# Performance work log

Measured on AMD Instinct MI355X. Metric: run time of the kernel, lower is better.

Reference implementation:

```python
import jax, jax.numpy as jnp
import numpy as np

N, F_IN, E = 50000, 256, 1000000
UNITS, HEADS, LAYERS, OUT = 32, 8, 2, 64
D = UNITS * HEADS  # 256


def setup_inputs() -> dict:
    key = jax.random.key(0)
    ks = jax.random.split(key, 12)
    node_states = jax.random.normal(ks[0], (1, N, F_IN), dtype=jnp.float32)
    # edges sorted by source column (required by the tf.repeat/bincount trick)
    src = jnp.sort(jax.random.randint(ks[1], (E,), 0, N, dtype=jnp.int32))
    dst = jax.random.randint(ks[2], (E,), 0, N, dtype=jnp.int32)
    edges = jnp.stack([src, dst], axis=-1)[None]  # [1, E, 2]
    edge_weights = jax.random.uniform(ks[3], (1, E), dtype=jnp.float32)
    pos_cls = jax.random.randint(ks[4], (1, 128), 0, N, dtype=jnp.int32)
    s = 0.05
    Wp = jax.random.normal(ks[5], (F_IN, D), dtype=jnp.float32) * s
    bp = jnp.zeros((D,), dtype=jnp.float32)
    Wk = jax.random.normal(ks[6], (LAYERS, HEADS, D, UNITS), dtype=jnp.float32) * s
    Wa = jax.random.normal(ks[7], (LAYERS, HEADS, 2 * UNITS, 1), dtype=jnp.float32) * s
    Wo = jax.random.normal(ks[8], (D, OUT), dtype=jnp.float32) * s
    bo = jnp.zeros((OUT,), dtype=jnp.float32)
    return {
        "node_states": node_states, "edges": edges, "edge_weights": edge_weights,
        "pos_cls": pos_cls, "Wp": Wp, "bp": bp, "Wk": Wk, "Wa": Wa,
        "Wo": Wo, "bo": bo,
    }


def _gat_head(x, src, dst, ew, W, a, n_nodes):
    xt = x @ W  # [N, U]
    # edge features: concat(src_feat, dst_feat) scaled by edge weight
    ef = jnp.concatenate([xt[src], xt[dst]], axis=-1) * ew[:, None]  # [E, 2U]
    s = jax.nn.leaky_relu((ef @ a)[:, 0], negative_slope=0.2)        # [E]
    s = jnp.exp(jnp.clip(s, -2.0, 2.0))
    ssum = jax.ops.segment_sum(s, src, num_segments=n_nodes)          # [N]
    norm = s / ssum[src]
    return jax.ops.segment_sum(xt[dst] * norm[:, None], src, num_segments=n_nodes)


def reference(node_states, edges, edge_weights, pos_cls, Wp, bp, Wk, Wa, Wo, bo):
    x0 = node_states[0]        # [N, F_in]
    e = edges[0]               # [E, 2]
    ew = edge_weights[0]       # [E]
    src, dst = e[:, 0], e[:, 1]
    n_nodes = x0.shape[0]
    x = jax.nn.relu(x0 @ Wp + bp)  # [N, D]
    n_layers, n_heads = Wk.shape[0], Wk.shape[1]
    for l in range(n_layers):
        heads = [_gat_head(x, src, dst, ew, Wk[l, h], Wa[l, h], n_nodes)
                 for h in range(n_heads)]
        mh = jax.nn.relu(jnp.concatenate(heads, axis=-1))  # [N, D]
        x = mh + x  # residual
    out = x @ Wo + bo
    return out[None]  # [1, N, OUT]
```

## Files before the change

### kernel.cpp

```cpp
#include <hip/hip_runtime.h>
#include <hip/hip_bf16.h>
#include <math.h>

#define N_NODES 50000
#define F_DIM 256
#define NE 1000000
#define N_HEADS 8
#define M_PAD 50048

typedef __attribute__((ext_vector_type(8))) short short8;
typedef __attribute__((ext_vector_type(4))) float floatx4;
typedef __attribute__((ext_vector_type(2))) float floatx2;

__device__ __forceinline__ void load16_lds(const void* g, void* l) {
    __builtin_amdgcn_global_load_lds(
        (const __attribute__((address_space(1))) unsigned int*)(unsigned long long)g,
        (__attribute__((address_space(3))) unsigned int*)(unsigned int)(unsigned long long)l,
        16, 0, 0);
}

__device__ __forceinline__ unsigned int pack2bf(float a, float b) {
    __hip_bfloat16 t0 = __float2bfloat16(a), t1 = __float2bfloat16(b);
    unsigned short u0, u1;
    __builtin_memcpy(&u0, &t0, 2);
    __builtin_memcpy(&u1, &t1, 2);
    return (unsigned int)u0 | ((unsigned int)u1 << 16);
}

__device__ __forceinline__ float bf_lo(unsigned int u) {
    return __uint_as_float(u << 16);
}
__device__ __forceinline__ float bf_hi(unsigned int u) {
    return __uint_as_float(u & 0xffff0000u);
}

__device__ __forceinline__ unsigned int pack4fp8(float x, float y, float z,
                                                 float w) {
    int v = __builtin_amdgcn_cvt_pk_fp8_f32(x, y, 0, false);
    v = __builtin_amdgcn_cvt_pk_fp8_f32(z, w, v, true);
    return (unsigned int)v;
}

__global__ __launch_bounds__(256) void prep_kernel(
    const float* __restrict__ node_states, const int* __restrict__ edges,
    const float* __restrict__ ew, const float* __restrict__ Wp,
    const float* __restrict__ Wk, const float* __restrict__ Wo,
    __hip_bfloat16* __restrict__ xt16, int2* __restrict__ edata,
    __hip_bfloat16* __restrict__ wpT, __hip_bfloat16* __restrict__ wkT,
    __hip_bfloat16* __restrict__ woT, int* __restrict__ row_start) {
    const int b = blockIdx.x;
    const int tid = threadIdx.x;
    if (b < 12500) {
        const size_t i = ((size_t)b * 256 + tid) * 4;
        const float4 v = *(const float4*)(node_states + i);
        uint2 pk;
        pk.x = pack2bf(v.x, v.y);
        pk.y = pack2bf(v.z, v.w);
        *(uint2*)((unsigned short*)xt16 + i) = pk;
    } else if (b < 16407) {
        const int e = (b - 12500) * 256 + tid;
        if (e < NE) {
            int2 d;
            d.x = edges[2 * e + 1];
            d.y = __float_as_int(ew[e]);
            edata[e] = d;
        }
    } else if (b < 17239) {
        const int wb = b - 16407;
        if (wb < 256) {
            int idx = wb * 256 + tid;
            int n = idx >> 8, k = idx & 255;
            wpT[idx] = __float2bfloat16(Wp[k * 256 + n]);
        } else if (wb < 768) {
            int idx = (wb - 256) * 256 + tid;
            int l = idx >> 16, n = (idx >> 8) & 255, k = idx & 255;
            int h = n >> 5, u = n & 31;
            wkT[idx] = __float2bfloat16(Wk[(((l * 8 + h) * 256) + k) * 32 + u]);
        } else {
            int idx = (wb - 768) * 256 + tid;
            int n = idx >> 8, k = idx & 255;
            woT[idx] = __float2bfloat16(Wo[k * 64 + n]);
        }
    } else {
        const int i = (b - 17239) * 256 + tid;
        if (i > N_NODES) return;
        if (i == N_NODES) { row_start[N_NODES] = NE; return; }
        int lo = 0, hi = NE;
        while (lo < hi) {
            int mid = (lo + hi) >> 1;
            if (edges[2 * mid] < i) lo = mid + 1; else hi = mid;
        }
        row_start[i] = lo;
    }
}

template <bool BIAS_RELU, bool FP8OUT>
__global__ __launch_bounds__(256) void gemm_mfma(
    const __hip_bfloat16* __restrict__ A16, const __hip_bfloat16* __restrict__ BT,
    const float* __restrict__ bias, void* __restrict__ Y) {
    __shared__ __align__(16) short lA[128 * 32];
    __shared__ __align__(16) short lB[128 * 32];
    const int tid = threadIdx.x;
    const int row0 = blockIdx.x * 128;
    const int n0 = blockIdx.y * 128;
    const int w = tid >> 6, l = tid & 63;
    const int wr = w >> 1, wc = w & 1;

    const __hip_bfloat16* gA = A16 + (size_t)(row0 + (tid >> 2)) * 256 + (tid & 3) * 8;
    const __hip_bfloat16* gB = BT + (size_t)(n0 + (tid >> 2)) * 256 + (tid & 3) * 8;
    short* dA = lA + tid * 8;
    short* dB = lB + tid * 8;

    floatx4 acc[4][4] = {};

    const short* pa = lA + (wr * 64 + (l & 15)) * 32 + (l >> 4) * 8;
    const short* pb = lB + (wc * 64 + (l & 15)) * 32 + (l >> 4) * 8;

    for (int kk = 0; kk < 8; ++kk) {
        const int ko = kk * 32;
        load16_lds(gA + ko, dA);
        load16_lds(gA + 64 * 256 + ko, dA + 256 * 8);
        load16_lds(gB + ko, dB);
        load16_lds(gB + 64 * 256 + ko, dB + 256 * 8);
        __syncthreads();
        short8 af[4], bf[4];
#pragma unroll
        for (int t = 0; t < 4; ++t) {
            af[t] = *(const short8*)(pa + t * 16 * 32);
            bf[t] = *(const short8*)(pb + t * 16 * 32);
        }
#pragma unroll
        for (int mt = 0; mt < 4; ++mt)
#pragma unroll
            for (int nt = 0; nt < 4; ++nt)
                acc[mt][nt] = __builtin_amdgcn_mfma_f32_16x16x32_bf16(
                    bf[nt], af[mt], acc[mt][nt], 0, 0, 0);
        __syncthreads();
    }

    const int m_base = row0 + wr * 64 + (l & 15);
    const int n_base = n0 + wc * 64 + ((l >> 4) << 2);
#pragma unroll
    for (int mt = 0; mt < 4; ++mt) {
        const int m = m_base + mt * 16;
        if (m >= N_NODES) continue;
#pragma unroll
        for (int nt = 0; nt < 4; ++nt) {
            const int n = n_base + nt * 16;
            floatx4 v = acc[mt][nt];
            if (BIAS_RELU) {
                const float4 bb = *(const float4*)(bias + n);
                v.x = fmaxf(v.x + bb.x, 0.f);
                v.y = fmaxf(v.y + bb.y, 0.f);
                v.z = fmaxf(v.z + bb.z, 0.f);
                v.w = fmaxf(v.w + bb.w, 0.f);
            }
            if constexpr (FP8OUT) {
                *((unsigned int*)Y + (((size_t)m << 8) + n >> 2)) =
                    pack4fp8(v.x, v.y, v.z, v.w);
            } else {
                uint2 pk;
                pk.x = pack2bf(v.x, v.y);
                pk.y = pack2bf(v.z, v.w);
                *(uint2*)((unsigned short*)Y + ((size_t)m << 8) + n) = pk;
            }
        }
    }
}

__global__ __launch_bounds__(256) void gemm_mfma_out(
    const __hip_bfloat16* __restrict__ A16, const __hip_bfloat16* __restrict__ BT,
    const float* __restrict__ bias, float* __restrict__ out) {
    __shared__ __align__(16) short lA[128 * 32];
    __shared__ __align__(16) short lB[64 * 32];
    const int tid = threadIdx.x;
    const int row0 = blockIdx.x * 128;
    const int w = tid >> 6, l = tid & 63;

    const __hip_bfloat16* gA = A16 + (size_t)(row0 + (tid >> 2)) * 256 + (tid & 3) * 8;
    const __hip_bfloat16* gB = BT + (size_t)(tid >> 2) * 256 + (tid & 3) * 8;
    short* dA = lA + tid * 8;
    short* dB = lB + tid * 8;

    floatx4 acc[2][4] = {};

    const short* pa = lA + (w * 32 + (l & 15)) * 32 + (l >> 4) * 8;
    const short* pb = lB + (l & 15) * 32 + (l >> 4) * 8;

    for (int kk = 0; kk < 8; ++kk) {
        const int ko = kk * 32;
        load16_lds(gA + ko, dA);
        load16_lds(gA + 64 * 256 + ko, dA + 256 * 8);
        load16_lds(gB + ko, dB);
        __syncthreads();
        short8 af[2], bf[4];
#pragma unroll
        for (int t = 0; t < 2; ++t) af[t] = *(const short8*)(pa + t * 16 * 32);
#pragma unroll
        for (int t = 0; t < 4; ++t) bf[t] = *(const short8*)(pb + t * 16 * 32);
#pragma unroll
        for (int mt = 0; mt < 2; ++mt)
#pragma unroll
            for (int nt = 0; nt < 4; ++nt)
                acc[mt][nt] = __builtin_amdgcn_mfma_f32_16x16x32_bf16(
                    bf[nt], af[mt], acc[mt][nt], 0, 0, 0);
        __syncthreads();
    }

    const int m_base = row0 + w * 32 + (l & 15);
    const int n_base = (l >> 4) << 2;
#pragma unroll
    for (int mt = 0; mt < 2; ++mt) {
        const int m = m_base + mt * 16;
        if (m >= N_NODES) continue;
#pragma unroll
        for (int nt = 0; nt < 4; ++nt) {
            const int n = n_base + nt * 16;
            const float4 bb = *(const float4*)(bias + n);
            floatx4 v = acc[mt][nt];
            float4 o = {v.x + bb.x, v.y + bb.y, v.z + bb.z, v.w + bb.w};
            *(float4*)(&out[(size_t)m * 64 + n]) = o;
        }
    }
}

__global__ __launch_bounds__(256) void alpha_kernel(
    const unsigned int* __restrict__ xt8, const float* __restrict__ Wa_l,
    float* __restrict__ a_src, float* __restrict__ a_dst) {
    const int tid = threadIdx.x;
    const int node =
        __builtin_amdgcn_readfirstlane(blockIdx.x * 4 + (tid >> 6));
    const int l = tid & 63;
    const int h = l >> 3;
    const unsigned int u = xt8[(size_t)node * 64 + l];
    const floatx2 f01 = __builtin_amdgcn_cvt_pk_f32_fp8(u, false);
    const floatx2 f23 = __builtin_amdgcn_cvt_pk_f32_fp8(u, true);
    const float4 wa = *(const float4*)(Wa_l + h * 64 + (l & 7) * 4);
    const float4 wb = *(const float4*)(Wa_l + h * 64 + 32 + (l & 7) * 4);
    float p1 = f01.x * wa.x + f01.y * wa.y + f23.x * wa.z + f23.y * wa.w;
    float p2 = f01.x * wb.x + f01.y * wb.y + f23.x * wb.z + f23.y * wb.w;
#pragma unroll
    for (int off = 4; off > 0; off >>= 1) {
        p1 += __shfl_down(p1, off, 8);
        p2 += __shfl_down(p2, off, 8);
    }
    if ((l & 7) == 0) {
        a_src[node * N_HEADS + h] = p1;
        a_dst[node * N_HEADS + h] = p2;
    }
}

__device__ __forceinline__ float edge_score(float asrc, float ad, float w) {
    float sp = (asrc + ad) * w;
    sp = (sp >= 0.f) ? sp : 0.2f * sp;
    sp = fminf(fmaxf(sp, -2.f), 2.f);
    return __expf(sp);
}

#define ACC8(u, s)                                               \
    {                                                            \
        const floatx2 f01 = __builtin_amdgcn_cvt_pk_f32_fp8(u, false); \
        const floatx2 f23 = __builtin_amdgcn_cvt_pk_f32_fp8(u, true);  \
        a0 = fmaf(f01.x, s, a0);                                 \
        a1 = fmaf(f01.y, s, a1);                                 \
        a2 = fmaf(f23.x, s, a2);                                 \
        a3 = fmaf(f23.y, s, a3);                                 \
    }

__global__ __launch_bounds__(256) void edge_kernel(
    const unsigned long long* __restrict__ edata,
    const int* __restrict__ row_start, const unsigned int* __restrict__ xt8,
    const float* __restrict__ a_src, const float* __restrict__ a_dst,
    __hip_bfloat16* __restrict__ xb16) {
    const int tid = threadIdx.x;
    const int node =
        __builtin_amdgcn_readfirstlane(blockIdx.x * 4 + (tid >> 6));
    const int l = tid & 63;
    const int h = l >> 3;
    const float asrc = a_src[node * N_HEADS + h];
    const int e0 = row_start[node], e1 = row_start[node + 1];

    unsigned long long* xrow =
        (unsigned long long*)((unsigned short*)xb16 + (size_t)node * 256 +
                              l * 4);
    const unsigned long long xin = __builtin_nontemporal_load(xrow);

    float a0 = 0.f, a1 = 0.f, a2 = 0.f, a3 = 0.f, ssum = 0.f;
    int e = e0;
    for (; e + 4 <= e1; e += 4) {
        const unsigned long long ed0 = __builtin_nontemporal_load(edata + e);
        const unsigned long long ed1 = __builtin_nontemporal_load(edata + e + 1);
        const unsigned long long ed2 = __builtin_nontemporal_load(edata + e + 2);
        const unsigned long long ed3 = __builtin_nontemporal_load(edata + e + 3);
        const int d0 = (int)(unsigned int)ed0;
        const int d1 = (int)(unsigned int)ed1;
        const int d2 = (int)(unsigned int)ed2;
        const int d3 = (int)(unsigned int)ed3;
        const float w0 = __uint_as_float((unsigned int)(ed0 >> 32));
        const float w1 = __uint_as_float((unsigned int)(ed1 >> 32));
        const float w2 = __uint_as_float((unsigned int)(ed2 >> 32));
        const float w3 = __uint_as_float((unsigned int)(ed3 >> 32));
        const float s0 = edge_score(asrc, a_dst[d0 * N_HEADS + h], w0);
        const float s1 = edge_score(asrc, a_dst[d1 * N_HEADS + h], w1);
        const float s2 = edge_score(asrc, a_dst[d2 * N_HEADS + h], w2);
        const float s3 = edge_score(asrc, a_dst[d3 * N_HEADS + h], w3);
        const unsigned int u0 = xt8[(size_t)d0 * 64 + l];
        const unsigned int u1 = xt8[(size_t)d1 * 64 + l];
        const unsigned int u2 = xt8[(size_t)d2 * 64 + l];
        const unsigned int u3 = xt8[(size_t)d3 * 64 + l];
        ACC8(u0, s0);
        ACC8(u1, s1);
        ACC8(u2, s2);
        ACC8(u3, s3);
        ssum += (s0 + s1) + (s2 + s3);
    }
    for (; e < e1; ++e) {
        const unsigned long long ed = __builtin_nontemporal_load(edata + e);
        const int d = (int)(unsigned int)ed;
        const float w = __uint_as_float((unsigned int)(ed >> 32));
        const float s = edge_score(asrc, a_dst[d * N_HEADS + h], w);
        const unsigned int u = xt8[(size_t)d * 64 + l];
        ACC8(u, s);
        ssum += s;
    }
    const float inv = (e1 > e0) ? 1.f / ssum : 0.f;
    const unsigned int xlo = (unsigned int)xin;
    const unsigned int xhi = (unsigned int)(xin >> 32);
    const float c0 = bf_lo(xlo) + fmaxf(a0 * inv, 0.f);
    const float c1 = bf_hi(xlo) + fmaxf(a1 * inv, 0.f);
    const float c2 = bf_lo(xhi) + fmaxf(a2 * inv, 0.f);
    const float c3 = bf_hi(xhi) + fmaxf(a3 * inv, 0.f);
    const unsigned long long pk =
        (unsigned long long)pack2bf(c0, c1) |
        ((unsigned long long)pack2bf(c2, c3) << 32);
    __builtin_nontemporal_store(pk, xrow);
}

extern "C" void kernel_launch(void* const* d_in, const int* in_sizes, int n_in,
                              void* d_out, int out_size, void* d_ws,
                              size_t ws_size, hipStream_t stream) {
    const float* node_states = (const float*)d_in[0];
    const int* edges = (const int*)d_in[1];
    const float* ew = (const float*)d_in[2];
    const float* Wp = (const float*)d_in[4];
    const float* bp = (const float*)d_in[5];
    const float* Wk = (const float*)d_in[6];
    const float* Wa = (const float*)d_in[7];
    const float* Wo = (const float*)d_in[8];
    const float* bo = (const float*)d_in[9];
    float* out = (float*)d_out;

    char* ws = (char*)d_ws;
    __hip_bfloat16* xb16 = (__hip_bfloat16*)ws; ws += (size_t)M_PAD * 256 * 2;
    __hip_bfloat16* xt16 = (__hip_bfloat16*)ws; ws += (size_t)M_PAD * 256 * 2;
    unsigned int* xt8 = (unsigned int*)ws;      ws += (size_t)M_PAD * 256;
    int2* edata = (int2*)ws;                    ws += (size_t)NE * 8;
    float* a_src = (float*)ws;                  ws += (size_t)N_NODES * N_HEADS * 4;
    float* a_dst = (float*)ws;                  ws += (size_t)N_NODES * N_HEADS * 4;
    __hip_bfloat16* wpT = (__hip_bfloat16*)ws;  ws += 65536 * 2;
    __hip_bfloat16* wkT = (__hip_bfloat16*)ws;  ws += 131072 * 2;
    __hip_bfloat16* woT = (__hip_bfloat16*)ws;  ws += 16384 * 2;
    int* row_st = (int*)ws;

    prep_kernel<<<17435, 256, 0, stream>>>(node_states, edges, ew, Wp, Wk, Wo,
                                           xt16, edata, wpT, wkT, woT, row_st);

    gemm_mfma<true, false><<<dim3((N_NODES + 127) / 128, 2), 256, 0, stream>>>(
        xt16, wpT, bp, xb16);

    gemm_mfma<false, true><<<dim3((N_NODES + 127) / 128, 2), 256, 0, stream>>>(
        xb16, wkT, nullptr, xt8);
    alpha_kernel<<<N_NODES / 4, 256, 0, stream>>>(xt8, Wa, a_src, a_dst);
    edge_kernel<<<N_NODES / 4, 256, 0, stream>>>(
        (const unsigned long long*)edata, row_st, xt8, a_src, a_dst, xb16);

    gemm_mfma<false, true><<<dim3((N_NODES + 127) / 128, 2), 256, 0, stream>>>(
        xb16, wkT + 65536, nullptr, xt8);
    alpha_kernel<<<N_NODES / 4, 256, 0, stream>>>(xt8, Wa + 512, a_src, a_dst);
    edge_kernel<<<N_NODES / 4, 256, 0, stream>>>(
        (const unsigned long long*)edata, row_st, xt8, a_src, a_dst, xb16);

    gemm_mfma_out<<<(N_NODES + 127) / 128, 256, 0, stream>>>(xb16, woT, bo, out);
}
```

Before: 306.8 us.

## Fuse attention logits into GEMM epilogue and split edge loop across half-waves

Removes the separate alpha kernel by computing per-head source and destination attention logits in the GEMM epilogue from fp32 accumulators, using cross-lane shuffles. The edge kernel now has each half-wave handle alternating groups of four edges, with every lane gathering 8 fp8 features (uint2) instead of 4. The two halves are combined with an xor shuffle. This drops one launch and one full read of xt8 per layer and doubles the edge-level parallelism per wave. The cost is extra epilogue work, predicated padding edges, and logits computed from unrounded accumulators instead of fp8 values, which slightly changes numerics.

New measurement: 314.4 us. +2.5%, slower.

```diff
diff --git a/kernel.cpp b/kernel.cpp
--- a/kernel.cpp
+++ b/kernel.cpp
@@ -11,6 +11,7 @@
 typedef __attribute__((ext_vector_type(8))) short short8;
 typedef __attribute__((ext_vector_type(4))) float floatx4;
 typedef __attribute__((ext_vector_type(2))) float floatx2;
+typedef __attribute__((ext_vector_type(4))) unsigned int uintx4;
 
 __device__ __forceinline__ void load16_lds(const void* g, void* l) {
     __builtin_amdgcn_global_load_lds(
@@ -94,10 +95,12 @@
     }
 }
 
-template <bool BIAS_RELU, bool FP8OUT>
+template <bool BIAS_RELU, bool FP8OUT, bool ALPHA>
 __global__ __launch_bounds__(256) void gemm_mfma(
     const __hip_bfloat16* __restrict__ A16, const __hip_bfloat16* __restrict__ BT,
-    const float* __restrict__ bias, void* __restrict__ Y) {
+    const float* __restrict__ bias, void* __restrict__ Y,
+    const float* __restrict__ Wa_l, float* __restrict__ a_srcO,
+    float* __restrict__ a_dstO) {
     __shared__ __align__(16) short lA[128 * 32];
     __shared__ __align__(16) short lB[128 * 32];
     const int tid = threadIdx.x;
@@ -156,13 +159,60 @@
                 v.w = fmaxf(v.w + bb.w, 0.f);
             }
             if constexpr (FP8OUT) {
-                *((unsigned int*)Y + (((size_t)m << 8) + n >> 2)) =
+                *((unsigned int*)Y + ((((size_t)m << 8) + n) >> 2)) =
                     pack4fp8(v.x, v.y, v.z, v.w);
             } else {
                 uint2 pk;
                 pk.x = pack2bf(v.x, v.y);
                 pk.y = pack2bf(v.z, v.w);
                 *(uint2*)((unsigned short*)Y + ((size_t)m << 8) + n) = pk;
+            }
+        }
+    }
+
+    if constexpr (ALPHA) {
+        const int lg = l >> 4;
+        float4 wS[2][2], wD[2][2];
+#pragma unroll
+        for (int hl = 0; hl < 2; ++hl) {
+            const int h = (n0 >> 5) + wc * 2 + hl;
+#pragma unroll
+            for (int p = 0; p < 2; ++p) {
+                wS[hl][p] = *(const float4*)(Wa_l + h * 64 + p * 16 + lg * 4);
+                wD[hl][p] =
+                    *(const float4*)(Wa_l + h * 64 + 32 + p * 16 + lg * 4);
+            }
+        }
+        float aS[4][2], aD[4][2];
+#pragma unroll
+        for (int mt = 0; mt < 4; ++mt)
+#pragma unroll
+            for (int hl = 0; hl < 2; ++hl) {
+                float s = 0.f, d = 0.f;
+#pragma unroll
+                for (int p = 0; p < 2; ++p) {
+                    const floatx4 v = acc[mt][2 * hl + p];
+                    const float4 ws = wS[hl][p], wd = wD[hl][p];
+                    s += v.x * ws.x + v.y * ws.y + v.z * ws.z + v.w * ws.w;
+                    d += v.x * wd.x + v.y * wd.y + v.z * wd.z + v.w * wd.w;
+                }
+                s += __shfl_xor(s, 16);
+                s += __shfl_xor(s, 32);
+                d += __shfl_xor(d, 16);
+                d += __shfl_xor(d, 32);
+                aS[mt][hl] = s;
+                aD[mt][hl] = d;
+            }
+        if (lg == 0) {
+#pragma unroll
+            for (int mt = 0; mt < 4; ++mt) {
+                const int m = m_base + mt * 16;
+#pragma unroll
+                for (int hl = 0; hl < 2; ++hl) {
+                    const int h = (n0 >> 5) + wc * 2 + hl;
+                    a_srcO[(size_t)m * 8 + h] = aS[mt][hl];
+                    a_dstO[(size_t)m * 8 + h] = aD[mt][hl];
+                }
             }
         }
     }
@@ -224,32 +274,6 @@
     }
 }
 
-__global__ __launch_bounds__(256) void alpha_kernel(
-    const unsigned int* __restrict__ xt8, const float* __restrict__ Wa_l,
-    float* __restrict__ a_src, float* __restrict__ a_dst) {
-    const int tid = threadIdx.x;
-    const int node =
-        __builtin_amdgcn_readfirstlane(blockIdx.x * 4 + (tid >> 6));
-    const int l = tid & 63;
-    const int h = l >> 3;
-    const unsigned int u = xt8[(size_t)node * 64 + l];
-    const floatx2 f01 = __builtin_amdgcn_cvt_pk_f32_fp8(u, false);
-    const floatx2 f23 = __builtin_amdgcn_cvt_pk_f32_fp8(u, true);
-    const float4 wa = *(const float4*)(Wa_l + h * 64 + (l & 7) * 4);
-    const float4 wb = *(const float4*)(Wa_l + h * 64 + 32 + (l & 7) * 4);
-    float p1 = f01.x * wa.x + f01.y * wa.y + f23.x * wa.z + f23.y * wa.w;
-    float p2 = f01.x * wb.x + f01.y * wb.y + f23.x * wb.z + f23.y * wb.w;
-#pragma unroll
-    for (int off = 4; off > 0; off >>= 1) {
-        p1 += __shfl_down(p1, off, 8);
-        p2 += __shfl_down(p2, off, 8);
-    }
-    if ((l & 7) == 0) {
-        a_src[node * N_HEADS + h] = p1;
-        a_dst[node * N_HEADS + h] = p2;
-    }
-}
-
 __device__ __forceinline__ float edge_score(float asrc, float ad, float w) {
     float sp = (asrc + ad) * w;
     sp = (sp >= 0.f) ? sp : 0.2f * sp;
@@ -257,83 +281,81 @@
     return __expf(sp);
 }
 
-#define ACC8(u, s)                                               \
-    {                                                            \
-        const floatx2 f01 = __builtin_amdgcn_cvt_pk_f32_fp8(u, false); \
-        const floatx2 f23 = __builtin_amdgcn_cvt_pk_f32_fp8(u, true);  \
-        a0 = fmaf(f01.x, s, a0);                                 \
-        a1 = fmaf(f01.y, s, a1);                                 \
-        a2 = fmaf(f23.x, s, a2);                                 \
-        a3 = fmaf(f23.y, s, a3);                                 \
-    }
-
 __global__ __launch_bounds__(256) void edge_kernel(
     const unsigned long long* __restrict__ edata,
-    const int* __restrict__ row_start, const unsigned int* __restrict__ xt8,
+    const int* __restrict__ row_start, const uint2* __restrict__ xt8v,
     const float* __restrict__ a_src, const float* __restrict__ a_dst,
     __hip_bfloat16* __restrict__ xb16) {
     const int tid = threadIdx.x;
     const int node =
         __builtin_amdgcn_readfirstlane(blockIdx.x * 4 + (tid >> 6));
-    const int l = tid & 63;
-    const int h = l >> 3;
+    const int lane = tid & 63;
+    const int half = lane >> 5;
+    const int c = lane & 31;
+    const int h = c >> 2;
+    const int e0 = row_start[node], e1 = row_start[node + 1];
     const float asrc = a_src[node * N_HEADS + h];
-    const int e0 = row_start[node], e1 = row_start[node + 1];
-
-    unsigned long long* xrow =
-        (unsigned long long*)((unsigned short*)xb16 + (size_t)node * 256 +
-                              l * 4);
-    const unsigned long long xin = __builtin_nontemporal_load(xrow);
-
-    float a0 = 0.f, a1 = 0.f, a2 = 0.f, a3 = 0.f, ssum = 0.f;
-    int e = e0;
-    for (; e + 4 <= e1; e += 4) {
-        const unsigned long long ed0 = __builtin_nontemporal_load(edata + e);
-        const unsigned long long ed1 = __builtin_nontemporal_load(edata + e + 1);
-        const unsigned long long ed2 = __builtin_nontemporal_load(edata + e + 2);
-        const unsigned long long ed3 = __builtin_nontemporal_load(edata + e + 3);
-        const int d0 = (int)(unsigned int)ed0;
-        const int d1 = (int)(unsigned int)ed1;
-        const int d2 = (int)(unsigned int)ed2;
-        const int d3 = (int)(unsigned int)ed3;
-        const float w0 = __uint_as_float((unsigned int)(ed0 >> 32));
-        const float w1 = __uint_as_float((unsigned int)(ed1 >> 32));
-        const float w2 = __uint_as_float((unsigned int)(ed2 >> 32));
-        const float w3 = __uint_as_float((unsigned int)(ed3 >> 32));
-        const float s0 = edge_score(asrc, a_dst[d0 * N_HEADS + h], w0);
-        const float s1 = edge_score(asrc, a_dst[d1 * N_HEADS + h], w1);
-        const float s2 = edge_score(asrc, a_dst[d2 * N_HEADS + h], w2);
-        const float s3 = edge_score(asrc, a_dst[d3 * N_HEADS + h], w3);
-        const unsigned int u0 = xt8[(size_t)d0 * 64 + l];
-        const unsigned int u1 = xt8[(size_t)d1 * 64 + l];
-        const unsigned int u2 = xt8[(size_t)d2 * 64 + l];
-        const unsigned int u3 = xt8[(size_t)d3 * 64 + l];
-        ACC8(u0, s0);
-        ACC8(u1, s1);
-        ACC8(u2, s2);
-        ACC8(u3, s3);
-        ssum += (s0 + s1) + (s2 + s3);
-    }
-    for (; e < e1; ++e) {
-        const unsigned long long ed = __builtin_nontemporal_load(edata + e);
-        const int d = (int)(unsigned int)ed;
-        const float w = __uint_as_float((unsigned int)(ed >> 32));
-        const float s = edge_score(asrc, a_dst[d * N_HEADS + h], w);
-        const unsigned int u = xt8[(size_t)d * 64 + l];
-        ACC8(u, s);
-        ssum += s;
-    }
+
+    float a0 = 0.f, a1 = 0.f, a2 = 0.f, a3 = 0.f;
+    float a4 = 0.f, a5 = 0.f, a6 = 0.f, a7 = 0.f, ssum = 0.f;
+    for (int eb = e0 + (half << 2); eb < e1; eb += 8) {
+#pragma unroll
+        for (int j = 0; j < 4; ++j) {
+            const int e = eb + j;
+            const bool valid = e < e1;
+            const int ec = valid ? e : (e1 - 1);
+            const unsigned long long ed =
+                __builtin_nontemporal_load(edata + ec);
+            const int d = (int)(unsigned int)ed;
+            const float w = __uint_as_float((unsigned int)(ed >> 32));
+            float s = edge_score(asrc, a_dst[d * N_HEADS + h], w);
+            s = valid ? s : 0.f;
+            const uint2 u = xt8v[(size_t)d * 32 + c];
+            const floatx2 f01 = __builtin_amdgcn_cvt_pk_f32_fp8(u.x, false);
+            const floatx2 f23 = __builtin_amdgcn_cvt_pk_f32_fp8(u.x, true);
+            const floatx2 f45 = __builtin_amdgcn_cvt_pk_f32_fp8(u.y, false);
+            const floatx2 f67 = __builtin_amdgcn_cvt_pk_f32_fp8(u.y, true);
+            a0 = fmaf(f01.x, s, a0);
+            a1 = fmaf(f01.y, s, a1);
+            a2 = fmaf(f23.x, s, a2);
+            a3 = fmaf(f23.y, s, a3);
+            a4 = fmaf(f45.x, s, a4);
+            a5 = fmaf(f45.y, s, a5);
+            a6 = fmaf(f67.x, s, a6);
+            a7 = fmaf(f67.y, s, a7);
+            ssum += s;
+        }
+    }
+    a0 += __shfl_xor(a0, 32);
+    a1 += __shfl_xor(a1, 32);
+    a2 += __shfl_xor(a2, 32);
+    a3 += __shfl_xor(a3, 32);
+    a4 += __shfl_xor(a4, 32);
+    a5 += __shfl_xor(a5, 32);
+    a6 += __shfl_xor(a6, 32);
+    a7 += __shfl_xor(a7, 32);
+    ssum += __shfl_xor(ssum, 32);
     const float inv = (e1 > e0) ? 1.f / ssum : 0.f;
-    const unsigned int xlo = (unsigned int)xin;
-    const unsigned int xhi = (unsigned int)(xin >> 32);
-    const float c0 = bf_lo(xlo) + fmaxf(a0 * inv, 0.f);
-    const float c1 = bf_hi(xlo) + fmaxf(a1 * inv, 0.f);
-    const float c2 = bf_lo(xhi) + fmaxf(a2 * inv, 0.f);
-    const float c3 = bf_hi(xhi) + fmaxf(a3 * inv, 0.f);
-    const unsigned long long pk =
-        (unsigned long long)pack2bf(c0, c1) |
-        ((unsigned long long)pack2bf(c2, c3) << 32);
-    __builtin_nontemporal_store(pk, xrow);
+
+    if (lane < 32) {
+        uintx4* xrow =
+            (uintx4*)((unsigned short*)xb16 + (size_t)node * 256 + c * 8);
+        const uintx4 xin = __builtin_nontemporal_load(xrow);
+        const float c0 = bf_lo(xin.x) + fmaxf(a0 * inv, 0.f);
+        const float c1 = bf_hi(xin.x) + fmaxf(a1 * inv, 0.f);
+        const float c2 = bf_lo(xin.y) + fmaxf(a2 * inv, 0.f);
+        const float c3 = bf_hi(xin.y) + fmaxf(a3 * inv, 0.f);
+        const float c4 = bf_lo(xin.z) + fmaxf(a4 * inv, 0.f);
+        const float c5 = bf_hi(xin.z) + fmaxf(a5 * inv, 0.f);
+        const float c6 = bf_lo(xin.w) + fmaxf(a6 * inv, 0.f);
+        const float c7 = bf_hi(xin.w) + fmaxf(a7 * inv, 0.f);
+        uintx4 pk;
+        pk.x = pack2bf(c0, c1);
+        pk.y = pack2bf(c2, c3);
+        pk.z = pack2bf(c4, c5);
+        pk.w = pack2bf(c6, c7);
+        __builtin_nontemporal_store(pk, xrow);
+    }
 }
 
 extern "C" void kernel_launch(void* const* d_in, const int* in_sizes, int n_in,
@@ -355,8 +377,8 @@
     __hip_bfloat16* xt16 = (__hip_bfloat16*)ws; ws += (size_t)M_PAD * 256 * 2;
     unsigned int* xt8 = (unsigned int*)ws;      ws += (size_t)M_PAD * 256;
     int2* edata = (int2*)ws;                    ws += (size_t)NE * 8;
-    float* a_src = (float*)ws;                  ws += (size_t)N_NODES * N_HEADS * 4;
-    float* a_dst = (float*)ws;                  ws += (size_t)N_NODES * N_HEADS * 4;
+    float* a_src = (float*)ws;                  ws += (size_t)M_PAD * N_HEADS * 4;
+    float* a_dst = (float*)ws;                  ws += (size_t)M_PAD * N_HEADS * 4;
     __hip_bfloat16* wpT = (__hip_bfloat16*)ws;  ws += 65536 * 2;
     __hip_bfloat16* wkT = (__hip_bfloat16*)ws;  ws += 131072 * 2;
     __hip_bfloat16* woT = (__hip_bfloat16*)ws;  ws += 16384 * 2;
@@ -365,20 +387,23 @@
     prep_kernel<<<17435, 256, 0, stream>>>(node_states, edges, ew, Wp, Wk, Wo,
                                            xt16, edata, wpT, wkT, woT, row_st);
 
-    gemm_mfma<true, false><<<dim3((N_NODES + 127) / 128, 2), 256, 0, stream>>>(
-        xt16, wpT, bp, xb16);
-
-    gemm_mfma<false, true><<<dim3((N_NODES + 127) / 128, 2), 256, 0, stream>>>(
-        xb16, wkT, nullptr, xt8);
-    alpha_kernel<<<N_NODES / 4, 256, 0, stream>>>(xt8, Wa, a_src, a_dst);
+    gemm_mfma<true, false, false><<<dim3((N_NODES + 127) / 128, 2), 256, 0,
+                                    stream>>>(xt16, wpT, bp, xb16, nullptr,
+                                              nullptr, nullptr);
+
+    gemm_mfma<false, true, true><<<dim3((N_NODES + 127) / 128, 2), 256, 0,
+                                   stream>>>(xb16, wkT, nullptr, xt8, Wa,
+                                             a_src, a_dst);
     edge_kernel<<<N_NODES / 4, 256, 0, stream>>>(
-        (const unsigned long long*)edata, row_st, xt8, a_src, a_dst, xb16);
-
-    gemm_mfma<false, true><<<dim3((N_NODES + 127) / 128, 2), 256, 0, stream>>>(
-        xb16, wkT + 65536, nullptr, xt8);
-    alpha_kernel<<<N_NODES / 4, 256, 0, stream>>>(xt8, Wa + 512, a_src, a_dst);
+        (const unsigned long long*)edata, row_st, (const uint2*)xt8, a_src,
+        a_dst, xb16);
+
+    gemm_mfma<false, true, true><<<dim3((N_NODES + 127) / 128, 2), 256, 0,
+                                   stream>>>(xb16, wkT + 65536, nullptr, xt8,
+                                             Wa + 512, a_src, a_dst);
     edge_kernel<<<N_NODES / 4, 256, 0, stream>>>(
-        (const unsigned long long*)edata, row_st, xt8, a_src, a_dst, xb16);
+        (const unsigned long long*)edata, row_st, (const uint2*)xt8, a_src,
+        a_dst, xb16);
 
     gemm_mfma_out<<<(N_NODES + 127) / 128, 256, 0, stream>>>(xb16, woT, bo, out);
 }
```
